# Performance work log

Measured on AMD Instinct MI355X. Metric: run time of the kernel, lower is better.

## Reference

```python
import jax, jax.numpy as jnp
import numpy as np

QMAX = 127.0  # int8 symmetric
EPS = 1e-8

def _quant_dequant(v, axis):
    # symmetric int8 fake-quant along `axis` (per-row for weights, per-token for acts)
    scale = jnp.max(jnp.abs(v), axis=axis, keepdims=True) / QMAX
    scale = jnp.maximum(scale, EPS)
    q = jnp.clip(jnp.round(v / scale), -QMAX, QMAX)
    return q * scale

def _ste(v, axis):
    # straight-through estimator: identity gradient through quantization
    return v + jax.lax.stop_gradient(_quant_dequant(v, axis) - v)

def setup_inputs() -> dict:
    key = jax.random.key(0)
    k1, k2, k3 = jax.random.split(key, 3)
    H, I = 2048, 5632
    x = jax.random.normal(k1, (4, 2048, H), dtype=jnp.float32)
    # nn.Linear weight layout: [out_features, in_features]
    w_gate_up = jax.random.normal(k2, (2 * I, H), dtype=jnp.float32) * (H ** -0.5)
    w_down = jax.random.normal(k3, (H, I), dtype=jnp.float32) * (I ** -0.5)
    return {"x": x, "w_gate_up": w_gate_up, "w_down": w_down}

def reference(x, w_gate_up, w_down):
    I = w_down.shape[1]
    # QLinear #1: quantize act per-token, weight per-out-channel, dequant matmul
    xq = _ste(x, axis=-1)                       # [B,S,H]
    w1q = _ste(w_gate_up, axis=-1)              # [2I,H]
    gate_up = jnp.einsum('bsh,oh->bso', xq, w1q)  # [B,S,2I]
    gate, up = gate_up[..., :I], gate_up[..., I:]
    h = jax.nn.silu(gate) * up                  # SwiGLU, [B,S,I]
    # QLinear #2
    hq = _ste(h, axis=-1)
    w2q = _ste(w_down, axis=-1)                 # [H,I]
    return jnp.einsum('bsi,oi->bso', hq, w2q)   # [B,S,H]
```

## Files before the change

### kernel.cpp

```cpp
#include <hip/hip_runtime.h>
#include <hip/hip_bf16.h>
#include <stdint.h>

#define H_DIM 2048
#define I_DIM 5632
#define M_DIM 8192
#define N1_DIM (2 * I_DIM)
#define NBN1 (I_DIM / 128)
#define NPART (NBN1 * 4)

typedef __attribute__((ext_vector_type(4))) int i32x4;

__device__ __forceinline__ void gload16(const void* g, void* l) {
  __builtin_amdgcn_global_load_lds(
      reinterpret_cast<const __attribute__((address_space(1))) uint32_t*>(
          reinterpret_cast<uintptr_t>(g)),
      reinterpret_cast<__attribute__((address_space(3))) uint32_t*>(
          reinterpret_cast<uintptr_t>(l)),
      16, 0, 0);
}

__device__ __forceinline__ i32x4 ds_read128(uint32_t addr) {
  i32x4 d;
  asm volatile("s_mov_b32 m0, -1\n\tds_read_b128 %0, %1"
               : "=v"(d)
               : "v"(addr));
  return d;
}

#define MEMF() asm volatile("" ::: "memory")
#define BAR()                      \
  do {                             \
    MEMF();                        \
    __builtin_amdgcn_s_barrier();  \
    MEMF();                        \
  } while (0)
#define SCHEDB() __builtin_amdgcn_sched_barrier(0)

__global__ __launch_bounds__(256) void quant_rows_f32(
    const float* __restrict__ in, int8_t* __restrict__ q,
    float* __restrict__ scl, int rowlen) {
  const int row = blockIdx.x;
  const int tid = threadIdx.x;
  const float* rp = in + (size_t)row * rowlen;
  float m = 0.f;
  for (int i = tid * 4; i < rowlen; i += 1024) {
    const float4 v = *reinterpret_cast<const float4*>(rp + i);
    m = fmaxf(m, fmaxf(fmaxf(fabsf(v.x), fabsf(v.y)),
                       fmaxf(fabsf(v.z), fabsf(v.w))));
  }
#pragma unroll
  for (int o = 32; o; o >>= 1) m = fmaxf(m, __shfl_xor(m, o));
  __shared__ float wm[4];
  if ((tid & 63) == 0) wm[tid >> 6] = m;
  __syncthreads();
  m = fmaxf(fmaxf(wm[0], wm[1]), fmaxf(wm[2], wm[3]));
  const float scale = fmaxf(m / 127.0f, 1e-8f);
  const float inv = 1.0f / scale;
  if (tid == 0) scl[row] = scale;
  int8_t* qp = q + (size_t)row * rowlen;
  for (int i = tid * 4; i < rowlen; i += 1024) {
    const float4 v = *reinterpret_cast<const float4*>(rp + i);
    const int a = (int)rintf(fminf(fmaxf(v.x * inv, -127.f), 127.f));
    const int b = (int)rintf(fminf(fmaxf(v.y * inv, -127.f), 127.f));
    const int c = (int)rintf(fminf(fmaxf(v.z * inv, -127.f), 127.f));
    const int d = (int)rintf(fminf(fmaxf(v.w * inv, -127.f), 127.f));
    *reinterpret_cast<int*>(qp + i) =
        (a & 255) | ((b & 255) << 8) | ((c & 255) << 16) | (d << 24);
  }
}

__global__ __launch_bounds__(256) void quant_h_rows(
    const __hip_bfloat16* __restrict__ h, const float* __restrict__ hpart,
    int8_t* __restrict__ q, float* __restrict__ scl) {
  const int row = blockIdx.x;
  const int tid = threadIdx.x;
  float m = (tid < NPART) ? hpart[(size_t)row * NPART + tid] : 0.f;
#pragma unroll
  for (int o = 32; o; o >>= 1) m = fmaxf(m, __shfl_xor(m, o));
  __shared__ float wm[4];
  if ((tid & 63) == 0) wm[tid >> 6] = m;
  __syncthreads();
  m = fmaxf(fmaxf(wm[0], wm[1]), fmaxf(wm[2], wm[3]));
  const float scale = fmaxf(m / 127.0f, 1e-8f);
  const float inv = 1.0f / scale;
  if (tid == 0) scl[row] = scale;
  const __hip_bfloat16* rp = h + (size_t)row * I_DIM;
  int8_t* qp = q + (size_t)row * I_DIM;
  for (int i = tid * 8; i < I_DIM; i += 2048) {
    const uint4 v = *reinterpret_cast<const uint4*>(rp + i);
    const uint32_t w[4] = {v.x, v.y, v.z, v.w};
    int pk0 = 0, pk1 = 0;
#pragma unroll
    for (int j = 0; j < 8; ++j) {
      const float f =
          __uint_as_float(((w[j >> 1] >> ((j & 1) * 16)) & 0xffffu) << 16);
      const int qv = (int)rintf(fminf(fmaxf(f * inv, -127.f), 127.f));
      if (j < 4) pk0 |= (qv & 255) << ((j & 3) * 8);
      else       pk1 |= (qv & 255) << ((j & 3) * 8);
    }
    *reinterpret_cast<int2*>(qp + i) = make_int2(pk0, pk1);
  }
}

#define RD_A(MH, BUF)                                                          \
  do {                                                                         \
    _Pragma("unroll") for (int m = 0; m < 4; ++m) {                            \
      a[MH][m][0] = ds_read128(aB0 + (BUF) + (MH)*16384 + m * 2048);           \
      a[MH][m][1] = ds_read128(aB1 + (BUF) + (MH)*16384 + m * 2048);           \
    }                                                                          \
  } while (0)

#define RD_B(NH, BUF)                                                          \
  do {                                                                         \
    _Pragma("unroll") for (int n = 0; n < 2; ++n) {                            \
      b[NH][n][0] = ds_read128(bB0 + (BUF) + (NH)*16384 + n * 2048);           \
      b[NH][n][1] = ds_read128(bB1 + (BUF) + (NH)*16384 + n * 2048);           \
    }                                                                          \
  } while (0)

#define MFMA_Q(MH, NH)                                                         \
  do {                                                                         \
    __builtin_amdgcn_s_setprio(1);                                             \
    _Pragma("unroll") for (int kk = 0; kk < 2; ++kk)                           \
        _Pragma("unroll") for (int m = 0; m < 4; ++m)                          \
            _Pragma("unroll") for (int n = 0; n < 2; ++n) acc[MH][m][NH][n] =  \
        __builtin_amdgcn_mfma_i32_16x16x64_i8(a[MH][m][kk], b[NH][n][kk],      \
                                              acc[MH][m][NH][n], 0, 0, 0);     \
    __builtin_amdgcn_s_setprio(0);                                             \
  } while (0)

#define KTILE_BODY(SA, SB)                                                     \
  do {                                                                         \
    const int cb = (t & 1) * 32768;                                            \
    const int nb = cb ^ 32768;                                                 \
                                                                      \
    SCHEDB();                                                                  \
    RD_B(1, cb);                                                               \
    MEMF();                                                                    \
    if (t + 1 < KT) SA(1, t + 1);                                              \
    asm volatile("s_waitcnt lgkmcnt(4)" ::: "memory");                         \
    SCHEDB();                                                                  \
    MFMA_Q(0, 0);                                                              \
    BAR();                                                                     \
                                                                      \
    SCHEDB();                                                                  \
    RD_A(1, cb);                                                               \
    MEMF();                                                                    \
    if (t + 1 < KT) SB(1, t + 1);                                              \
    asm volatile("s_waitcnt lgkmcnt(8)" ::: "memory");                         \
    SCHEDB();                                                                  \
    MFMA_Q(0, 1);                                                              \
    BAR();                                                                     \
                                                                      \
    SCHEDB();                                                                  \
    if (t + 2 < KT) SA(0, t + 2);                                              \
    asm volatile("s_waitcnt lgkmcnt(0)" ::: "memory");                         \
    SCHEDB();                                                                  \
    MFMA_Q(1, 0);                                                              \
    if (t + 2 < KT) asm volatile("s_waitcnt vmcnt(6)" ::: "memory");           \
    else            asm volatile("s_waitcnt vmcnt(0)" ::: "memory");           \
    BAR();                                                                     \
                                                                      \
    SCHEDB();                                                                  \
    if (t + 1 < KT) { RD_A(0, nb); RD_B(0, nb); }                              \
    MEMF();                                                                    \
    if (t + 2 < KT) SB(0, t + 2);                                              \
    MFMA_Q(1, 1);                                                              \
    if (t + 1 < KT) {                                                          \
      if (t + 2 < KT) asm volatile("s_waitcnt vmcnt(4)" ::: "memory");         \
      else            asm volatile("s_waitcnt vmcnt(0)" ::: "memory");         \
    }                                                                          \
    BAR();                                                                     \
  } while (0)

__global__ __launch_bounds__(512, 2) void gemm1_silu(
    const int8_t* __restrict__ qx, const float* __restrict__ sx,
    const int8_t* __restrict__ qw, const float* __restrict__ sw,
    __hip_bfloat16* __restrict__ h, float* __restrict__ hpart) {
  __shared__ int8_t lds[131072];
  const int tid = threadIdx.x;
  const int lane = tid & 63;
  const int wid = tid >> 6;
  const int wr = wid >> 2, wc = wid & 3;
  const int c16 = lane & 15, kq = lane >> 4, r7 = lane & 7, lr = lane >> 3;
  const int sslot = ((lane & 7) ^ lr) << 4;
  const int sl0 = (kq ^ r7) << 4;
  const int sl1 = ((4 + kq) ^ r7) << 4;

  const int nwg = gridDim.x;
  const int id = blockIdx.x;
  const int swz = (id & 7) * (nwg >> 3) + (id >> 3);
  const int bm = swz / NBN1, bn = swz % NBN1;

  const int xrow = wid * 8 + lr;
  const int fx = (xrow & ~31) | ((xrow & 15) << 1) | ((xrow >> 4) & 1);

  const size_t goffA = (size_t)(bm * 256 + xrow) * H_DIM + sslot;
  const size_t goffG = (size_t)(bn * 128 + fx) * H_DIM + sslot;
  const size_t goffU = goffG + (size_t)I_DIM * H_DIM;
  const int ldsAw = wid * 8 * 128;
  const int ldsBw = 65536 + wid * 8 * 128;

  const uint32_t L = (uint32_t)(uintptr_t)(void*)&lds[0];
  const uint32_t aB0 = L + (wr * 64 + c16) * 128 + sl0;
  const uint32_t aB1 = L + (wr * 64 + c16) * 128 + sl1;
  const uint32_t bB0 = L + 65536 + (wc * 32 + c16) * 128 + sl0;
  const uint32_t bB1 = L + 65536 + (wc * 32 + c16) * 128 + sl1;

  i32x4 acc[2][4][2][2] = {};
  i32x4 a[2][4][2], b[2][2][2];

#define STAGE_A1(half, t)                                                      \
  do {                                                                         \
    const int _b = ((t) & 1) * 32768;                                          \
    _Pragma("unroll") for (int ld = 0; ld < 2; ++ld)                           \
        gload16(qx + goffA + (size_t)((half)*128 + ld * 64) * H_DIM +          \
                    (size_t)(t) * 128,                                         \
                lds + _b + ldsAw + ((half)*128 + ld * 64) * 128);              \
  } while (0)

#define STAGE_B1(half, t)                                                      \
  do {                                                                         \
    const int _b = ((t) & 1) * 32768;                                          \
    const int8_t* _s = (half) ? (qw + goffU) : (qw + goffG);                   \
    _Pragma("unroll") for (int ld = 0; ld < 2; ++ld)                           \
        gload16(_s + (size_t)(ld * 64) * H_DIM + (size_t)(t) * 128,            \
                lds + _b + ldsBw + ((half)*128 + ld * 64) * 128);              \
  } while (0)

  const int KT = H_DIM / 128;
  STAGE_A1(0, 0); STAGE_B1(0, 0); STAGE_A1(1, 0); STAGE_B1(1, 0);
  STAGE_A1(0, 1); STAGE_B1(0, 1);
  asm volatile("s_waitcnt vmcnt(4)" ::: "memory");
  BAR();
  RD_A(0, 0); RD_B(0, 0);
  MEMF();

#pragma unroll 1
  for (int t = 0; t < KT; ++t) {
    KTILE_BODY(STAGE_A1, STAGE_B1);
  }

  const int row0 = bm * 256 + wr * 64 + kq * 4;
  const int colb = bn * 128 + wc * 32 + 2 * c16;
#pragma unroll
  for (int mh = 0; mh < 2; ++mh) {
#pragma unroll
    for (int m = 0; m < 4; ++m) {
#pragma unroll
      for (int r = 0; r < 4; ++r) {
        const int row = row0 + mh * 128 + m * 16 + r;
        const float sxr = sx[row];
        float hv[2];
#pragma unroll
        for (int n = 0; n < 2; ++n) {
          const int col = colb + n;
          const float g = (float)acc[mh][m][0][n][r] * (sxr * sw[col]);
          const float u = (float)acc[mh][m][1][n][r] * (sxr * sw[I_DIM + col]);
          hv[n] = g / (1.f + __expf(-g)) * u;
        }
        const uint32_t p0 = __bfloat16_as_ushort(__float2bfloat16(hv[0]));
        const uint32_t p1 = __bfloat16_as_ushort(__float2bfloat16(hv[1]));
        *reinterpret_cast<uint32_t*>(&h[(size_t)row * I_DIM + colb]) =
            p0 | (p1 << 16);
        float rmax = fmaxf(fabsf(hv[0]), fabsf(hv[1]));
#pragma unroll
        for (int o = 1; o < 16; o <<= 1)
          rmax = fmaxf(rmax, __shfl_xor(rmax, o));
        if (c16 == 0)
          hpart[(size_t)row * NPART + bn * 4 + wc] = rmax;
      }
    }
  }
}

__global__ __launch_bounds__(512, 2) void gemm2(
    const int8_t* __restrict__ qh, const float* __restrict__ sh,
    const int8_t* __restrict__ qw, const float* __restrict__ sw,
    float* __restrict__ out) {
  __shared__ int8_t lds[131072];
  const int tid = threadIdx.x;
  const int lane = tid & 63;
  const int wid = tid >> 6;
  const int wr = wid >> 2, wc = wid & 3;
  const int c16 = lane & 15, kq = lane >> 4, r7 = lane & 7, lr = lane >> 3;
  const int sslot = ((lane & 7) ^ lr) << 4;
  const int sl0 = (kq ^ r7) << 4;
  const int sl1 = ((4 + kq) ^ r7) << 4;

  const int nwg = gridDim.x;
  const int id = blockIdx.x;
  const int swz = (id & 7) * (nwg >> 3) + (id >> 3);
  const int NBN = H_DIM / 256;
  const int bm = swz / NBN, bn = swz % NBN;

  const size_t goffA = (size_t)(bm * 256 + wid * 8 + lr) * I_DIM + sslot;
  const size_t goffB = (size_t)(bn * 256 + wid * 8 + lr) * I_DIM + sslot;
  const int ldsAw = wid * 8 * 128;
  const int ldsBw = 65536 + wid * 8 * 128;

  const uint32_t L = (uint32_t)(uintptr_t)(void*)&lds[0];
  const uint32_t aB0 = L + (wr * 64 + c16) * 128 + sl0;
  const uint32_t aB1 = L + (wr * 64 + c16) * 128 + sl1;
  const uint32_t bB0 = L + 65536 + (wc * 32 + c16) * 128 + sl0;
  const uint32_t bB1 = L + 65536 + (wc * 32 + c16) * 128 + sl1;

  i32x4 acc[2][4][2][2] = {};
  i32x4 a[2][4][2], b[2][2][2];

#define STAGE_A2(half, t)                                                      \
  do {                                                                         \
    const int _b = ((t) & 1) * 32768;                                          \
    _Pragma("unroll") for (int ld = 0; ld < 2; ++ld)                           \
        gload16(qh + goffA + (size_t)((half)*128 + ld * 64) * I_DIM +          \
                    (size_t)(t) * 128,                                         \
                lds + _b + ldsAw + ((half)*128 + ld * 64) * 128);              \
  } while (0)

#define STAGE_B2(half, t)                                                      \
  do {                                                                         \
    const int _b = ((t) & 1) * 32768;                                          \
    _Pragma("unroll") for (int ld = 0; ld < 2; ++ld)                           \
        gload16(qw + goffB + (size_t)((half)*128 + ld * 64) * I_DIM +          \
                    (size_t)(t) * 128,                                         \
                lds + _b + ldsBw + ((half)*128 + ld * 64) * 128);              \
  } while (0)

  const int KT = I_DIM / 128;
  STAGE_A2(0, 0); STAGE_B2(0, 0); STAGE_A2(1, 0); STAGE_B2(1, 0);
  STAGE_A2(0, 1); STAGE_B2(0, 1);
  asm volatile("s_waitcnt vmcnt(4)" ::: "memory");
  BAR();
  RD_A(0, 0); RD_B(0, 0);
  MEMF();

#pragma unroll 1
  for (int t = 0; t < KT; ++t) {
    KTILE_BODY(STAGE_A2, STAGE_B2);
  }

  const int row0 = bm * 256 + wr * 64 + kq * 4;
  const int col0 = bn * 256 + wc * 32 + c16;
#pragma unroll
  for (int mh = 0; mh < 2; ++mh) {
#pragma unroll
    for (int m = 0; m < 4; ++m) {
#pragma unroll
      for (int r = 0; r < 4; ++r) {
        const int row = row0 + mh * 128 + m * 16 + r;
        const float shr = sh[row];
#pragma unroll
        for (int nh = 0; nh < 2; ++nh) {
#pragma unroll
          for (int n = 0; n < 2; ++n) {
            const int col = col0 + nh * 128 + n * 16;
            out[(size_t)row * H_DIM + col] =
                (float)acc[mh][m][nh][n][r] * (shr * sw[col]);
          }
        }
      }
    }
  }
}

extern "C" void kernel_launch(void* const* d_in, const int* in_sizes, int n_in,
                              void* d_out, int out_size, void* d_ws, size_t ws_size,
                              hipStream_t stream) {
  (void)in_sizes; (void)n_in; (void)out_size; (void)ws_size;
  const float* x  = (const float*)d_in[0];
  const float* w1 = (const float*)d_in[1];
  const float* w2 = (const float*)d_in[2];
  float* out = (float*)d_out;

  size_t off = 0;
  auto alloc = [&](size_t n) {
    void* p = (char*)d_ws + off;
    off += (n + 255) & ~(size_t)255;
    return p;
  };
  int8_t* qx  = (int8_t*)alloc((size_t)M_DIM * H_DIM);
  int8_t* qw1 = (int8_t*)alloc((size_t)N1_DIM * H_DIM);
  int8_t* qw2 = (int8_t*)alloc((size_t)H_DIM * I_DIM);
  int8_t* qh  = (int8_t*)alloc((size_t)M_DIM * I_DIM);
  __hip_bfloat16* hb = (__hip_bfloat16*)alloc((size_t)M_DIM * I_DIM * 2);
  float* sx    = (float*)alloc((size_t)M_DIM * 4);
  float* sw1   = (float*)alloc((size_t)N1_DIM * 4);
  float* sw2   = (float*)alloc((size_t)H_DIM * 4);
  float* shs   = (float*)alloc((size_t)M_DIM * 4);
  float* hpart = (float*)alloc((size_t)M_DIM * NPART * 4);

  quant_rows_f32<<<M_DIM, 256, 0, stream>>>(x, qx, sx, H_DIM);
  quant_rows_f32<<<N1_DIM, 256, 0, stream>>>(w1, qw1, sw1, H_DIM);
  quant_rows_f32<<<H_DIM, 256, 0, stream>>>(w2, qw2, sw2, I_DIM);
  gemm1_silu<<<(M_DIM / 256) * NBN1, 512, 0, stream>>>(
      qx, sx, qw1, sw1, hb, hpart);
  quant_h_rows<<<M_DIM, 256, 0, stream>>>(hb, hpart, qh, shs);
  gemm2<<<(M_DIM / 256) * (H_DIM / 256), 512, 0, stream>>>(
      qh, shs, qw2, sw2, out);
}
```

Measured before the change: 403.3 us.

## Halve gemm1 K-tile to 64 and LDS to 64KB for four blocks per CU

The first int8 GEMM's K-tile drops from 128 to 64 bytes, which halves LDS to 64KB and lets launch bounds ask for 4 blocks of 512 threads per CU instead of 2. The fine-grained four-phase pipeline with register double-buffered fragments is replaced by a simpler two-phase loop: read A-half and B, run MFMAs, read the second A-half, barrier, issue the next global prefetch, run MFMAs. The swizzle changes to a 4-slot XOR for the 64-byte rows. It trades more barriers per K and less intra-wave overlap for higher occupancy, and the tighter register budget at 4 blocks of 512 threads may cause spilling.

```diff
diff --git a/kernel.cpp b/kernel.cpp
--- a/kernel.cpp
+++ b/kernel.cpp
@@ -27,6 +27,11 @@
                : "v"(addr));
   return d;
 }
+
+#define DSR(dst, base, off)                                                    \
+  asm volatile("s_mov_b32 m0, -1\n\tds_read_b128 %0, %1 offset:" off           \
+               : "=v"(dst)                                                     \
+               : "v"(base))
 
 #define MEMF() asm volatile("" ::: "memory")
 #define BAR()                      \
@@ -134,7 +139,6 @@
   do {                                                                         \
     const int cb = (t & 1) * 32768;                                            \
     const int nb = cb ^ 32768;                                                 \
-                                                                      \
     SCHEDB();                                                                  \
     RD_B(1, cb);                                                               \
     MEMF();                                                                    \
@@ -143,7 +147,6 @@
     SCHEDB();                                                                  \
     MFMA_Q(0, 0);                                                              \
     BAR();                                                                     \
-                                                                      \
     SCHEDB();                                                                  \
     RD_A(1, cb);                                                               \
     MEMF();                                                                    \
@@ -152,7 +155,6 @@
     SCHEDB();                                                                  \
     MFMA_Q(0, 1);                                                              \
     BAR();                                                                     \
-                                                                      \
     SCHEDB();                                                                  \
     if (t + 2 < KT) SA(0, t + 2);                                              \
     asm volatile("s_waitcnt lgkmcnt(0)" ::: "memory");                         \
@@ -161,7 +163,6 @@
     if (t + 2 < KT) asm volatile("s_waitcnt vmcnt(6)" ::: "memory");           \
     else            asm volatile("s_waitcnt vmcnt(0)" ::: "memory");           \
     BAR();                                                                     \
-                                                                      \
     SCHEDB();                                                                  \
     if (t + 1 < KT) { RD_A(0, nb); RD_B(0, nb); }                              \
     MEMF();                                                                    \
@@ -174,72 +175,101 @@
     BAR();                                                                     \
   } while (0)
 
-__global__ __launch_bounds__(512, 2) void gemm1_silu(
+#define RD1_A0() do { DSR(a0[0], aA, "0");    DSR(a0[1], aA, "1024");          \
+                      DSR(a0[2], aA, "2048"); DSR(a0[3], aA, "3072"); } while (0)
+#define RD1_A1() do { DSR(a1[0], aA, "8192"); DSR(a1[1], aA, "9216");          \
+                      DSR(a1[2], aA, "10240"); DSR(a1[3], aA, "11264"); } while (0)
+#define RD1_B()  do { DSR(b0[0], bA, "0");    DSR(b0[1], bA, "1024");          \
+                      DSR(b1[0], bA, "8192"); DSR(b1[1], bA, "9216"); } while (0)
+
+#define MFMA_H(MH, AV)                                                         \
+  do {                                                                         \
+    __builtin_amdgcn_s_setprio(1);                                             \
+    _Pragma("unroll") for (int m = 0; m < 4; ++m) {                            \
+      _Pragma("unroll") for (int n = 0; n < 2; ++n) {                          \
+        acc[MH][m][0][n] = __builtin_amdgcn_mfma_i32_16x16x64_i8(              \
+            AV[m], b0[n], acc[MH][m][0][n], 0, 0, 0);                          \
+        acc[MH][m][1][n] = __builtin_amdgcn_mfma_i32_16x16x64_i8(              \
+            AV[m], b1[n], acc[MH][m][1][n], 0, 0, 0);                          \
+      }                                                                        \
+    }                                                                          \
+    __builtin_amdgcn_s_setprio(0);                                             \
+  } while (0)
+
+__global__ __launch_bounds__(512, 4) void gemm1_silu(
     const int8_t* __restrict__ qx, const float* __restrict__ sx,
     const int8_t* __restrict__ qw, const float* __restrict__ sw,
     __hip_bfloat16* __restrict__ h, float* __restrict__ hpart) {
-  __shared__ int8_t lds[131072];
+  __shared__ int8_t lds[65536];
   const int tid = threadIdx.x;
   const int lane = tid & 63;
   const int wid = tid >> 6;
   const int wr = wid >> 2, wc = wid & 3;
-  const int c16 = lane & 15, kq = lane >> 4, r7 = lane & 7, lr = lane >> 3;
-  const int sslot = ((lane & 7) ^ lr) << 4;
-  const int sl0 = (kq ^ r7) << 4;
-  const int sl1 = ((4 + kq) ^ r7) << 4;
+  const int c16 = lane & 15, kq = lane >> 4;
 
   const int nwg = gridDim.x;
   const int id = blockIdx.x;
   const int swz = (id & 7) * (nwg >> 3) + (id >> 3);
   const int bm = swz / NBN1, bn = swz % NBN1;
 
-  const int xrow = wid * 8 + lr;
+  const int srow = lane >> 2;
+  const int sslot16 = ((lane & 3) ^ (srow & 3)) << 4;
+  const int xrow = wid * 16 + srow;
   const int fx = (xrow & ~31) | ((xrow & 15) << 1) | ((xrow >> 4) & 1);
 
-  const size_t goffA = (size_t)(bm * 256 + xrow) * H_DIM + sslot;
-  const size_t goffG = (size_t)(bn * 128 + fx) * H_DIM + sslot;
-  const size_t goffU = goffG + (size_t)I_DIM * H_DIM;
-  const int ldsAw = wid * 8 * 128;
-  const int ldsBw = 65536 + wid * 8 * 128;
+  const size_t goffA = (size_t)(bm * 256 + xrow) * H_DIM + sslot16;
+  const size_t goffB = (size_t)(bn * 128 + fx) * H_DIM + sslot16;
 
   const uint32_t L = (uint32_t)(uintptr_t)(void*)&lds[0];
-  const uint32_t aB0 = L + (wr * 64 + c16) * 128 + sl0;
-  const uint32_t aB1 = L + (wr * 64 + c16) * 128 + sl1;
-  const uint32_t bB0 = L + 65536 + (wc * 32 + c16) * 128 + sl0;
-  const uint32_t bB1 = L + 65536 + (wc * 32 + c16) * 128 + sl1;
+  const uint32_t aBase = L + (wr * 64 + c16) * 64 + ((kq ^ (c16 & 3)) << 4);
+  const uint32_t bBase =
+      L + 32768 + (wc * 32 + c16) * 64 + ((kq ^ (c16 & 3)) << 4);
+
+#define STG1_A(t)                                                              \
+  do {                                                                         \
+    const int _cb = ((t) & 1) * 16384;                                         \
+    gload16(qx + goffA + (size_t)(t) * 64, lds + _cb + wid * 1024);            \
+    gload16(qx + goffA + (size_t)128 * H_DIM + (size_t)(t) * 64,               \
+            lds + _cb + 8192 + wid * 1024);                                    \
+  } while (0)
+
+#define STG1_B(t)                                                              \
+  do {                                                                         \
+    const int _cb = ((t) & 1) * 16384;                                         \
+    gload16(qw + goffB + (size_t)(t) * 64, lds + 32768 + _cb + wid * 1024);    \
+    gload16(qw + goffB + (size_t)I_DIM * H_DIM + (size_t)(t) * 64,             \
+            lds + 32768 + _cb + 8192 + wid * 1024);                            \
+  } while (0)
 
   i32x4 acc[2][4][2][2] = {};
-  i32x4 a[2][4][2], b[2][2][2];
-
-#define STAGE_A1(half, t)                                                      \
-  do {                                                                         \
-    const int _b = ((t) & 1) * 32768;                                          \
-    _Pragma("unroll") for (int ld = 0; ld < 2; ++ld)                           \
-        gload16(qx + goffA + (size_t)((half)*128 + ld * 64) * H_DIM +          \
-                    (size_t)(t) * 128,                                         \
-                lds + _b + ldsAw + ((half)*128 + ld * 64) * 128);              \
-  } while (0)
-
-#define STAGE_B1(half, t)                                                      \
-  do {                                                                         \
-    const int _b = ((t) & 1) * 32768;                                          \
-    const int8_t* _s = (half) ? (qw + goffU) : (qw + goffG);                   \
-    _Pragma("unroll") for (int ld = 0; ld < 2; ++ld)                           \
-        gload16(_s + (size_t)(ld * 64) * H_DIM + (size_t)(t) * 128,            \
-                lds + _b + ldsBw + ((half)*128 + ld * 64) * 128);              \
-  } while (0)
-
-  const int KT = H_DIM / 128;
-  STAGE_A1(0, 0); STAGE_B1(0, 0); STAGE_A1(1, 0); STAGE_B1(1, 0);
-  STAGE_A1(0, 1); STAGE_B1(0, 1);
+
+  const int KT = H_DIM / 64;
+  STG1_A(0); STG1_B(0);
+  STG1_A(1); STG1_B(1);
   asm volatile("s_waitcnt vmcnt(4)" ::: "memory");
   BAR();
-  RD_A(0, 0); RD_B(0, 0);
-  MEMF();
 
 #pragma unroll 1
   for (int t = 0; t < KT; ++t) {
-    KTILE_BODY(STAGE_A1, STAGE_B1);
+    const int cb = (t & 1) * 16384;
+    const uint32_t aA = aBase + cb;
+    const uint32_t bA = bBase + cb;
+    i32x4 a0[4], a1[4], b0[2], b1[2];
+    RD1_A0();
+    RD1_B();
+    asm volatile("s_waitcnt lgkmcnt(0)" ::: "memory");
+    SCHEDB();
+    MFMA_H(0, a0);
+    RD1_A1();
+    asm volatile("s_waitcnt lgkmcnt(0)" ::: "memory");
+    SCHEDB();
+    BAR();
+    if (t + 2 < KT) { STG1_A(t + 2); STG1_B(t + 2); }
+    MEMF();
+    MFMA_H(1, a1);
+    if (t + 2 < KT)      asm volatile("s_waitcnt vmcnt(4)" ::: "memory");
+    else if (t + 1 < KT) asm volatile("s_waitcnt vmcnt(0)" ::: "memory");
+    BAR();
   }
 
   const int row0 = bm * 256 + wr * 64 + kq * 4;
```

After: 1.578 ms. 3.91x slower.
